# Performance work log

Measured on AMD Instinct MI355X. Metric: run time of the kernel, lower is better.

## Reference

```python
import jax, jax.numpy as jnp
import numpy as np

D = 1024; NHEAD = 8; NQ = 256; B = 8; HM = 64; WM = 64; S = HM * WM; FF = 4 * D
EPS_LN = 1e-5


def _ln(x, g, b):
    m = x.mean(-1, keepdims=True)
    v = ((x - m) ** 2).mean(-1, keepdims=True)
    return (x - m) / jnp.sqrt(v + EPS_LN) * g + b


def _self_attn(x, w_in, b_in, w_out, b_out, nhead):
    # x: [L, B, D] (torch MultiheadAttention, batch_first=False, eval mode)
    L, Bn, Dm = x.shape
    hd = Dm // nhead
    qkv = x @ w_in.T + b_in  # [L, B, 3D]
    q, k, v = jnp.split(qkv, 3, axis=-1)
    sp = lambda t: t.reshape(L, Bn, nhead, hd).transpose(1, 2, 0, 3)  # [B, H, L, hd]
    q, k, v = sp(q), sp(k), sp(v)
    attn = jax.nn.softmax(jnp.einsum('bhqd,bhkd->bhqk', q, k) / float(hd) ** 0.5, axis=-1)
    out = jnp.einsum('bhqk,bhkd->bhqd', attn, v)
    out = out.transpose(2, 0, 1, 3).reshape(L, Bn, Dm)
    return out @ w_out.T + b_out


def setup_inputs() -> dict:
    key = jax.random.key(0)
    ks = iter(jax.random.split(key, 40))
    nrm = lambda shape: jax.random.normal(next(ks), shape, jnp.float32) * 0.02
    return dict(
        query=jax.random.normal(next(ks), (NQ, B, D), jnp.float32),
        memory=jax.random.normal(next(ks), (S, B, D), jnp.float32),
        prev_mask=jax.random.uniform(next(ks), (B, NQ, HM, WM), dtype=jnp.float32),
        h_mem=HM, w_mem=WM,
        sa_in_w=nrm((3 * D, D)), sa_in_b=jnp.zeros((3 * D,), jnp.float32),
        sa_out_w=nrm((D, D)), sa_out_b=jnp.zeros((D,), jnp.float32),
        ln1_g=jnp.ones((D,), jnp.float32), ln1_b=jnp.zeros((D,), jnp.float32),
        ln2_g=jnp.ones((D,), jnp.float32), ln2_b=jnp.zeros((D,), jnp.float32),
        ln3_g=jnp.ones((D,), jnp.float32), ln3_b=jnp.zeros((D,), jnp.float32),
        wq=nrm((D, D)), bq=jnp.zeros((D,), jnp.float32),
        wk=nrm((D, D)), bk=jnp.zeros((D,), jnp.float32),
        wv=nrm((D, D)), bv=jnp.zeros((D,), jnp.float32),
        wo=nrm((D, D)), bo=jnp.zeros((D,), jnp.float32),
        w1=nrm((FF, D)), b1=jnp.zeros((FF,), jnp.float32),
        w2=nrm((D, FF)), b2=jnp.zeros((D,), jnp.float32),
        mask_w=nrm((S, D)), mask_b=jnp.zeros((S,), jnp.float32),
    )


def reference(query, memory, prev_mask, h_mem, w_mem,
              sa_in_w, sa_in_b, sa_out_w, sa_out_b,
              ln1_g, ln1_b, ln2_g, ln2_b, ln3_g, ln3_b,
              wq, bq, wk, bk, wv, bv, wo, bo,
              w1, b1, w2, b2, mask_w, mask_b):
    nq, Bn, d_model = query.shape
    # --- self attention block ---
    q_norm = _ln(query, ln1_g, ln1_b)
    q2 = _self_attn(q_norm, sa_in_w, sa_in_b, sa_out_w, sa_out_b, NHEAD)
    query = query + q2
    # --- masked cross attention (single-head, as in source) ---
    Q = (_ln(query, ln2_g, ln2_b) @ wq.T + bq).transpose(1, 0, 2)  # [B, NQ, D]
    K = (memory @ wk.T + bk).transpose(1, 0, 2)                    # [B, S, D]
    V = (memory @ wv.T + bv).transpose(1, 0, 2)                    # [B, S, D]
    scores = jnp.einsum('bqd,bsd->bqs', Q, K) / float(d_model) ** 0.5
    scores = scores + jnp.log(prev_mask.reshape(Bn, nq, -1) + 1e-6)
    attn = jax.nn.softmax(scores, axis=-1)
    attn_out = jnp.einsum('bqs,bsd->bqd', attn, V).transpose(1, 0, 2)  # [NQ, B, D]
    query = query + (attn_out @ wo.T + bo)
    # --- FFN ---
    h = jax.nn.gelu(_ln(query, ln3_g, ln3_b) @ w1.T + b1, approximate=False)
    query = query + (h @ w2.T + b2)
    # --- mask prediction ---
    q_for_mask = query.transpose(1, 0, 2)                # [B, NQ, D]
    mask_logits = q_for_mask @ mask_w.T + mask_b          # [B, NQ, H*W]
    pred_mask = jax.nn.sigmoid(mask_logits.reshape(Bn, nq, h_mem, w_mem))
    return (query, pred_mask)
```

## Files before the change

### kernel.cpp

```cpp
#include <hip/hip_runtime.h>
#include <cstdint>


typedef __attribute__((ext_vector_type(8))) __bf16 bf16x8;
typedef __attribute__((ext_vector_type(4))) float f32x4;
typedef __attribute__((ext_vector_type(8))) unsigned short ushort8;
typedef __attribute__((ext_vector_type(4))) unsigned short ushort4v;

__device__ __forceinline__ unsigned short f2bf(float f) {
  return __builtin_bit_cast(unsigned short, (__bf16)f);
}

__global__ __launch_bounds__(256) void cast_bf16_kernel(const float* __restrict__ in,
                                                        unsigned short* __restrict__ out,
                                                        int n8) {
  int i = blockIdx.x * 256 + threadIdx.x;
  if (i >= n8) return;
  const float4* p = (const float4*)in + (size_t)i * 2;
  float4 a = p[0], b = p[1];
  ushort8 o;
  o[0] = f2bf(a.x); o[1] = f2bf(a.y); o[2] = f2bf(a.z); o[3] = f2bf(a.w);
  o[4] = f2bf(b.x); o[5] = f2bf(b.y); o[6] = f2bf(b.z); o[7] = f2bf(b.w);
  ((ushort8*)out)[i] = o;
}

__global__ __launch_bounds__(256) void ln_bf16_kernel(const float* __restrict__ x,
                                                      const float* __restrict__ g,
                                                      const float* __restrict__ b,
                                                      unsigned short* __restrict__ out) {
  int row = blockIdx.x, tid = threadIdx.x;
  const float4* xr = (const float4*)(x + (size_t)row * 1024);
  float4 v = xr[tid];
  float s = v.x + v.y + v.z + v.w;
  float sq = v.x * v.x + v.y * v.y + v.z * v.z + v.w * v.w;
#pragma unroll
  for (int o = 32; o > 0; o >>= 1) { s += __shfl_xor(s, o); sq += __shfl_xor(sq, o); }
  __shared__ float red[8];
  int wave = tid >> 6, lane = tid & 63;
  if (lane == 0) { red[wave] = s; red[4 + wave] = sq; }
  __syncthreads();
  float ts = red[0] + red[1] + red[2] + red[3];
  float tq = red[4] + red[5] + red[6] + red[7];
  float mean = ts * (1.f / 1024.f);
  float var = tq * (1.f / 1024.f) - mean * mean;
  float rstd = rsqrtf(var + 1e-5f);
  float4 gv = ((const float4*)g)[tid];
  float4 bv = ((const float4*)b)[tid];
  ushort4v o;
  o[0] = f2bf((v.x - mean) * rstd * gv.x + bv.x);
  o[1] = f2bf((v.y - mean) * rstd * gv.y + bv.y);
  o[2] = f2bf((v.z - mean) * rstd * gv.z + bv.z);
  o[3] = f2bf((v.w - mean) * rstd * gv.w + bv.w);
  ((ushort4v*)(out + (size_t)row * 1024))[tid] = o;
}

template <bool MASK, int CNT>
__global__ __launch_bounds__(256) void softmax_bf16_kernel(const float* __restrict__ sc,
                                                           const float* __restrict__ pm,
                                                           unsigned short* __restrict__ out,
                                                           float scale) {
  const int L = CNT * 256;
  int row = blockIdx.x, tid = threadIdx.x;
  const float* sr = sc + (size_t)row * L;
  float vals[CNT];
  float mx = -1e30f;
#pragma unroll
  for (int i = 0; i < CNT; i++) {
    int idx = tid + (i << 8);
    float v = sr[idx] * scale;
    if (MASK) v += __logf(pm[(size_t)row * L + idx] + 1e-6f);
    vals[i] = v;
    mx = fmaxf(mx, v);
  }
#pragma unroll
  for (int o = 32; o > 0; o >>= 1) mx = fmaxf(mx, __shfl_xor(mx, o));
  __shared__ float red[8];
  int wave = tid >> 6, lane = tid & 63;
  if (lane == 0) red[wave] = mx;
  __syncthreads();
  mx = fmaxf(fmaxf(red[0], red[1]), fmaxf(red[2], red[3]));
  float sum = 0.f;
#pragma unroll
  for (int i = 0; i < CNT; i++) { vals[i] = __expf(vals[i] - mx); sum += vals[i]; }
#pragma unroll
  for (int o = 32; o > 0; o >>= 1) sum += __shfl_xor(sum, o);
  if (lane == 0) red[4 + wave] = sum;
  __syncthreads();
  float rs = 1.f / (red[4] + red[5] + red[6] + red[7]);
#pragma unroll
  for (int i = 0; i < CNT; i++)
    out[(size_t)row * L + tid + (i << 8)] = f2bf(vals[i] * rs);
}

__global__ __launch_bounds__(256) void transpose_bf16_kernel(
    const unsigned short* __restrict__ in, unsigned short* __restrict__ out,
    long in_off, int in_rs, long in_hi, long in_lo, int zdiv,
    long out_off, int out_rs, long out_hi, long out_lo) {
  __shared__ unsigned short t[32][33];
  int z = blockIdx.z;
  int zh = z / zdiv, zl = z % zdiv;
  const unsigned short* ib = in + in_off + (long)zh * in_hi + (long)zl * in_lo;
  unsigned short* ob = out + out_off + (long)zh * out_hi + (long)zl * out_lo;
  int i0 = blockIdx.x * 32;
  int j0 = blockIdx.y * 32;
  int tx = threadIdx.x & 31, ty = threadIdx.x >> 5;
#pragma unroll
  for (int r = ty; r < 32; r += 8) t[r][tx] = ib[(long)(j0 + r) * in_rs + i0 + tx];
  __syncthreads();
#pragma unroll
  for (int r = ty; r < 32; r += 8) ob[(long)(i0 + r) * out_rs + j0 + tx] = t[tx][r];
}

template <bool AF32, bool BIAS, int ACT, bool RES, bool OUTF, bool OUTB>
__global__ __launch_bounds__(256) void gemm_nt_kernel(
    const void* __restrict__ Av, long a_off, int lda, long a_hi, long a_lo,
    const unsigned short* __restrict__ B, long b_off, int ldb, long b_hi, long b_lo,
    const float* __restrict__ bias, const float* __restrict__ Res,
    float* __restrict__ Cf, long c_off, int ldc, long c_hi, long c_lo,
    unsigned short* __restrict__ Cb, long cb_off, int ldcb, long cb_hi, long cb_lo,
    int K, int zdiv) {
  __shared__ unsigned short As[128 * 32];
  __shared__ unsigned short Bs[128 * 32];
  int tid = threadIdx.x;
  int wave = tid >> 6, lane = tid & 63;
  int z = blockIdx.z, zh = z / zdiv, zl = z % zdiv;
  long m0 = (long)blockIdx.x * 128, n0 = (long)blockIdx.y * 128;

  const unsigned short* Bb = B + b_off + zh * b_hi + zl * b_lo + n0 * ldb;
  const unsigned short* Ab16 = nullptr;
  const float* Abf = nullptr;
  if constexpr (AF32)
    Abf = (const float*)Av + a_off + zh * a_hi + zl * a_lo + m0 * lda;
  else
    Ab16 = (const unsigned short*)Av + a_off + zh * a_hi + zl * a_lo + m0 * lda;

  int srow = lane >> 2;
  int scol = (lane & 3) * 8;
  int wm = (wave >> 1) * 64, wn = (wave & 1) * 64;
  int fr = lane & 15;
  int ko = (lane >> 4) * 8;

  f32x4 acc[4][4] = {};

  for (int k0 = 0; k0 < K; k0 += 32) {
    __syncthreads();
    if constexpr (AF32) {
      int row = tid >> 1;
      int cs = (tid & 1) * 16;
      const float* ap = Abf + (long)row * lda + k0 + cs;
      float4 f0 = ((const float4*)ap)[0];
      float4 f1 = ((const float4*)ap)[1];
      float4 f2 = ((const float4*)ap)[2];
      float4 f3 = ((const float4*)ap)[3];
      ushort8 u0, u1;
      u0[0] = f2bf(f0.x); u0[1] = f2bf(f0.y); u0[2] = f2bf(f0.z); u0[3] = f2bf(f0.w);
      u0[4] = f2bf(f1.x); u0[5] = f2bf(f1.y); u0[6] = f2bf(f1.z); u0[7] = f2bf(f1.w);
      u1[0] = f2bf(f2.x); u1[1] = f2bf(f2.y); u1[2] = f2bf(f2.z); u1[3] = f2bf(f2.w);
      u1[4] = f2bf(f3.x); u1[5] = f2bf(f3.y); u1[6] = f2bf(f3.z); u1[7] = f2bf(f3.w);
      ushort8* dst = (ushort8*)(As + row * 32 + cs);
      dst[0] = u0;
      dst[1] = u1;
    } else {
#pragma unroll
      for (int is = 0; is < 2; is++) {
        int rbase = wave * 32 + is * 16;
        const unsigned short* g = Ab16 + (long)(rbase + srow) * lda + k0 + scol;
        __builtin_amdgcn_global_load_lds(
            (const __attribute__((address_space(1))) unsigned int*)g,
            (__attribute__((address_space(3))) unsigned int*)(As + rbase * 32), 16, 0, 0);
      }
    }
#pragma unroll
    for (int is = 0; is < 2; is++) {
      int rbase = wave * 32 + is * 16;
      const unsigned short* g = Bb + (long)(rbase + srow) * ldb + k0 + scol;
      __builtin_amdgcn_global_load_lds(
          (const __attribute__((address_space(1))) unsigned int*)g,
          (__attribute__((address_space(3))) unsigned int*)(Bs + rbase * 32), 16, 0, 0);
    }
    __syncthreads();

    bf16x8 af[4], bfv[4];
#pragma unroll
    for (int i = 0; i < 4; i++)
      af[i] = *(const bf16x8*)(As + (wm + i * 16 + fr) * 32 + ko);
#pragma unroll
    for (int j = 0; j < 4; j++)
      bfv[j] = *(const bf16x8*)(Bs + (wn + j * 16 + fr) * 32 + ko);
#pragma unroll
    for (int i = 0; i < 4; i++)
#pragma unroll
      for (int j = 0; j < 4; j++)
        acc[i][j] = __builtin_amdgcn_mfma_f32_16x16x32_bf16(af[i], bfv[j], acc[i][j], 0, 0, 0);
  }

  long cfo = c_off + zh * c_hi + zl * c_lo;
  long cbo = cb_off + zh * cb_hi + zl * cb_lo;
  int rq = (lane >> 4) * 4;
#pragma unroll
  for (int i = 0; i < 4; i++) {
    long rbase = m0 + wm + i * 16 + rq;
#pragma unroll
    for (int j = 0; j < 4; j++) {
      long cc = n0 + wn + j * 16 + fr;
      float bsv = BIAS ? bias[cc] : 0.f;
#pragma unroll
      for (int r = 0; r < 4; r++) {
        float v = acc[i][j][r] + bsv;
        long ro = rbase + r;
        if constexpr (RES) v += Res[cfo + ro * ldc + cc];
        if constexpr (ACT == 1) v = 0.5f * v * (1.f + erff(v * 0.7071067811865475f));
        if constexpr (ACT == 2) v = 1.f / (1.f + __expf(-v));
        if constexpr (OUTF) Cf[cfo + ro * ldc + cc] = v;
        if constexpr (OUTB) Cb[cbo + ro * ldcb + cc] = f2bf(v);
      }
    }
  }
}

template <bool AF32, bool BIAS, int ACT, bool RES, bool OUTF, bool OUTB>
static void launch_gemm(hipStream_t s, int M, int N, int K, int nz, int zdiv,
                        const void* A, long a_off, int lda, long a_hi, long a_lo,
                        const unsigned short* B, long b_off, int ldb, long b_hi, long b_lo,
                        const float* bias, const float* Res,
                        float* Cf, long c_off, int ldc, long c_hi, long c_lo,
                        unsigned short* Cb, long cb_off, int ldcb, long cb_hi, long cb_lo) {
  dim3 g(M / 128, N / 128, nz);
  gemm_nt_kernel<AF32, BIAS, ACT, RES, OUTF, OUTB><<<g, dim3(256), 0, s>>>(
      A, a_off, lda, a_hi, a_lo, B, b_off, ldb, b_hi, b_lo, bias, Res,
      Cf, c_off, ldc, c_hi, c_lo, Cb, cb_off, ldcb, cb_hi, cb_lo, K, zdiv);
}

static const long WB_SAIN = 0;
static const long WB_SAOUT = 6291456;
static const long WB_WQ = 8388608;
static const long WB_WK = 10485760;
static const long WB_WV = 12582912;
static const long WB_WO = 14680064;
static const long WB_W1 = 16777216;
static const long WB_W2 = 25165824;
static const long WB_MW = 33554432;
static const long OF_K = 41943040;
static const long OF_V = 109051904;
static const long OF_QKV = 176160768;
static const long OF_SC = 188743680;
static const long OF_P = 222298112;
static const long OF_QN = 239075328;
static const long OF_Q = 243269632;
static const long OF_CTX = 247463936;

extern "C" void kernel_launch(void* const* d_in, const int* in_sizes, int n_in,
                              void* d_out, int out_size, void* d_ws, size_t ws_size,
                              hipStream_t stream) {
  (void)in_sizes; (void)n_in; (void)out_size; (void)ws_size;
  const float* query = (const float*)d_in[0];
  const float* memoryp = (const float*)d_in[1];
  const float* prev_mask = (const float*)d_in[2];
  const float* sa_in_w = (const float*)d_in[5];
  const float* sa_in_b = (const float*)d_in[6];
  const float* sa_out_w = (const float*)d_in[7];
  const float* sa_out_b = (const float*)d_in[8];
  const float* ln1_g = (const float*)d_in[9], * ln1_b = (const float*)d_in[10];
  const float* ln2_g = (const float*)d_in[11], * ln2_b = (const float*)d_in[12];
  const float* ln3_g = (const float*)d_in[13], * ln3_b = (const float*)d_in[14];
  const float* wq = (const float*)d_in[15], * bq = (const float*)d_in[16];
  const float* wk = (const float*)d_in[17], * bk = (const float*)d_in[18];
  const float* wv = (const float*)d_in[19], * bv = (const float*)d_in[20];
  const float* wo = (const float*)d_in[21], * bo = (const float*)d_in[22];
  const float* w1 = (const float*)d_in[23], * b1 = (const float*)d_in[24];
  const float* w2 = (const float*)d_in[25], * b2 = (const float*)d_in[26];
  const float* mask_w = (const float*)d_in[27], * mask_b = (const float*)d_in[28];

  uint8_t* ws = (uint8_t*)d_ws;
  auto bf = [&](long off) { return (unsigned short*)(ws + off); };
  auto fp = [&](long off) { return (float*)(ws + off); };
  unsigned short* ZB = nullptr;
  float* ZF = nullptr;

  auto cast = [&](const float* src, long dst, int n) {
    int n8 = n / 8;
    cast_bf16_kernel<<<dim3((n8 + 255) / 256), dim3(256), 0, stream>>>(src, bf(dst), n8);
  };

  cast(sa_in_w, WB_SAIN, 3072 * 1024);
  cast(sa_out_w, WB_SAOUT, 1024 * 1024);
  cast(wq, WB_WQ, 1024 * 1024);
  cast(wk, WB_WK, 1024 * 1024);
  cast(wv, WB_WV, 1024 * 1024);
  cast(wo, WB_WO, 1024 * 1024);
  cast(w1, WB_W1, 4096 * 1024);
  cast(w2, WB_W2, 1024 * 4096);
  cast(mask_w, WB_MW, 4096 * 1024);

  ln_bf16_kernel<<<2048, 256, 0, stream>>>(query, ln1_g, ln1_b, bf(OF_QN));

  launch_gemm<false, true, 0, false, false, true>(stream, 2048, 3072, 1024, 1, 1,
      bf(OF_QN), 0, 1024, 0, 0, bf(WB_SAIN), 0, 1024, 0, 0, sa_in_b, nullptr,
      ZF, 0, 0, 0, 0, bf(OF_QKV), 0, 3072, 0, 0);

  launch_gemm<false, false, 0, false, true, false>(stream, 256, 256, 128, 64, 8,
      bf(OF_QKV), 0, 24576, 3072, 128,
      bf(OF_QKV), 1024, 24576, 3072, 128, nullptr, nullptr,
      fp(OF_SC), 0, 256, 524288, 65536, ZB, 0, 0, 0, 0);

  softmax_bf16_kernel<false, 1><<<16384, 256, 0, stream>>>(
      fp(OF_SC), nullptr, bf(OF_P), 0.08838834764831845f);

  transpose_bf16_kernel<<<dim3(4, 8, 64), 256, 0, stream>>>(
      bf(OF_QKV), bf(OF_QN), 2048L, 24576, 3072L, 128L, 8, 0L, 256, 262144L, 32768L);

  launch_gemm<false, false, 0, false, false, true>(stream, 256, 128, 256, 64, 8,
      bf(OF_P), 0, 256, 524288, 65536,
      bf(OF_QN), 0, 256, 262144, 32768, nullptr, nullptr,
      ZF, 0, 0, 0, 0, bf(OF_CTX), 0, 8192, 1024, 128);

  launch_gemm<false, true, 0, true, true, false>(stream, 2048, 1024, 1024, 1, 1,
      bf(OF_CTX), 0, 1024, 0, 0, bf(WB_SAOUT), 0, 1024, 0, 0, sa_out_b, query,
      fp(OF_QKV), 0, 1024, 0, 0, ZB, 0, 0, 0, 0);

  ln_bf16_kernel<<<2048, 256, 0, stream>>>(fp(OF_QKV), ln2_g, ln2_b, bf(OF_QN));

  launch_gemm<false, true, 0, false, false, true>(stream, 2048, 1024, 1024, 1, 1,
      bf(OF_QN), 0, 1024, 0, 0, bf(WB_WQ), 0, 1024, 0, 0, bq, nullptr,
      ZF, 0, 0, 0, 0, bf(OF_Q), 0, 1024, 0, 0);

  launch_gemm<true, true, 0, false, false, true>(stream, 32768, 1024, 1024, 1, 1,
      memoryp, 0, 1024, 0, 0, bf(WB_WK), 0, 1024, 0, 0, bk, nullptr,
      ZF, 0, 0, 0, 0, bf(OF_K), 0, 1024, 0, 0);
  launch_gemm<true, true, 0, false, false, true>(stream, 32768, 1024, 1024, 1, 1,
      memoryp, 0, 1024, 0, 0, bf(WB_WV), 0, 1024, 0, 0, bv, nullptr,
      ZF, 0, 0, 0, 0, bf(OF_V), 0, 1024, 0, 0);

  launch_gemm<false, false, 0, false, true, false>(stream, 256, 4096, 1024, 8, 1,
      bf(OF_Q), 0, 8192, 1024, 0,
      bf(OF_K), 0, 8192, 1024, 0, nullptr, nullptr,
      fp(OF_SC), 0, 4096, 1048576, 0, ZB, 0, 0, 0, 0);

  softmax_bf16_kernel<true, 16><<<2048, 256, 0, stream>>>(
      fp(OF_SC), prev_mask, bf(OF_P), 0.03125f);

  transpose_bf16_kernel<<<dim3(32, 128, 8), 256, 0, stream>>>(
      bf(OF_V), bf(OF_K), 0L, 8192, 1024L, 0L, 1, 0L, 4096, 4194304L, 0L);

  launch_gemm<false, false, 0, false, false, true>(stream, 256, 1024, 4096, 8, 1,
      bf(OF_P), 0, 4096, 1048576, 0,
      bf(OF_K), 0, 4096, 4194304, 0, nullptr, nullptr,
      ZF, 0, 0, 0, 0, bf(OF_CTX), 0, 8192, 1024, 0);

  launch_gemm<false, true, 0, true, true, false>(stream, 2048, 1024, 1024, 1, 1,
      bf(OF_CTX), 0, 1024, 0, 0, bf(WB_WO), 0, 1024, 0, 0, bo, fp(OF_QKV),
      fp(OF_SC), 0, 1024, 0, 0, ZB, 0, 0, 0, 0);

  ln_bf16_kernel<<<2048, 256, 0, stream>>>(fp(OF_SC), ln3_g, ln3_b, bf(OF_QN));

  launch_gemm<false, true, 1, false, false, true>(stream, 2048, 4096, 1024, 1, 1,
      bf(OF_QN), 0, 1024, 0, 0, bf(WB_W1), 0, 1024, 0, 0, b1, nullptr,
      ZF, 0, 0, 0, 0, bf(OF_P), 0, 4096, 0, 0);

  launch_gemm<false, true, 0, true, true, true>(stream, 2048, 1024, 4096, 1, 1,
      bf(OF_P), 0, 4096, 0, 0, bf(WB_W2), 0, 4096, 0, 0, b2, fp(OF_SC),
      (float*)d_out, 0, 1024, 0, 0, bf(OF_CTX), 0, 1024, 0, 0);

  launch_gemm<false, true, 2, false, true, false>(stream, 256, 4096, 1024, 8, 1,
      bf(OF_CTX), 0, 8192, 1024, 0,
      bf(WB_MW), 0, 1024, 0, 0, mask_b, nullptr,
      (float*)d_out + 2097152, 0, 4096, 1048576, 0, ZB, 0, 0, 0, 0);
}
```

Measured before the change: 1.123 ms.

## Fuse K/V projections, batch weight casts, pre-cast memory, add 64-row GEMM tiles

Replaces the nine weight-cast launches with a single multi-segment cast kernel. The separate K and V projections become one GEMM with N=2048 over concatenated WK|WV weights and a concatenated bias, with the epilogue splitting columns into the K and V buffers. When the workspace is large enough, memory is pre-cast to bf16 so that GEMM can use async global-to-LDS loads instead of converting fp32 in the loop. GEMMs with N=1024 or small grids switch to a 64-row M tile to raise block count. The trade-off is extra workspace, one more pass over memory, and lower per-block reuse on the 64-row tiles.

```diff
diff --git a/kernel.cpp b/kernel.cpp
--- a/kernel.cpp
+++ b/kernel.cpp
@@ -22,6 +22,31 @@
   o[0] = f2bf(a.x); o[1] = f2bf(a.y); o[2] = f2bf(a.z); o[3] = f2bf(a.w);
   o[4] = f2bf(b.x); o[5] = f2bf(b.y); o[6] = f2bf(b.z); o[7] = f2bf(b.w);
   ((ushort8*)out)[i] = o;
+}
+
+struct CastSegs {
+  const float* src[9];
+  int cum[10];
+};
+__global__ __launch_bounds__(256) void cast_multi_kernel(CastSegs cs,
+                                                         unsigned short* __restrict__ out) {
+  int i = blockIdx.x * 256 + threadIdx.x;
+  if (i >= cs.cum[9]) return;
+  int s = 0;
+  while (i >= cs.cum[s + 1]) s++;
+  const float4* p = (const float4*)cs.src[s] + (size_t)(i - cs.cum[s]) * 2;
+  float4 a = p[0], b = p[1];
+  ushort8 o;
+  o[0] = f2bf(a.x); o[1] = f2bf(a.y); o[2] = f2bf(a.z); o[3] = f2bf(a.w);
+  o[4] = f2bf(b.x); o[5] = f2bf(b.y); o[6] = f2bf(b.z); o[7] = f2bf(b.w);
+  ((ushort8*)out)[i] = o;
+}
+
+__global__ __launch_bounds__(256) void bias_concat_kernel(const float* __restrict__ a,
+                                                          const float* __restrict__ b,
+                                                          float* __restrict__ o) {
+  int i = blockIdx.x * 256 + threadIdx.x;
+  o[i] = i < 1024 ? a[i] : b[i - 1024];
 }
 
 __global__ __launch_bounds__(256) void ln_bf16_kernel(const float* __restrict__ x,
@@ -111,7 +136,7 @@
   for (int r = ty; r < 32; r += 8) ob[(long)(i0 + r) * out_rs + j0 + tx] = t[tx][r];
 }
 
-template <bool AF32, bool BIAS, int ACT, bool RES, bool OUTF, bool OUTB>
+template <int TM, bool AF32, bool BIAS, int ACT, bool RES, bool OUTF, bool OUTB, bool KVSPLIT>
 __global__ __launch_bounds__(256) void gemm_nt_kernel(
     const void* __restrict__ Av, long a_off, int lda, long a_hi, long a_lo,
     const unsigned short* __restrict__ B, long b_off, int ldb, long b_hi, long b_lo,
@@ -119,12 +144,13 @@
     float* __restrict__ Cf, long c_off, int ldc, long c_hi, long c_lo,
     unsigned short* __restrict__ Cb, long cb_off, int ldcb, long cb_hi, long cb_lo,
     int K, int zdiv) {
-  __shared__ unsigned short As[128 * 32];
+  constexpr int MI = TM / 32;
+  __shared__ unsigned short As[TM * 32];
   __shared__ unsigned short Bs[128 * 32];
   int tid = threadIdx.x;
   int wave = tid >> 6, lane = tid & 63;
   int z = blockIdx.z, zh = z / zdiv, zl = z % zdiv;
-  long m0 = (long)blockIdx.x * 128, n0 = (long)blockIdx.y * 128;
+  long m0 = (long)blockIdx.x * TM, n0 = (long)blockIdx.y * 128;
 
   const unsigned short* Bb = B + b_off + zh * b_hi + zl * b_lo + n0 * ldb;
   const unsigned short* Ab16 = nullptr;
@@ -136,11 +162,11 @@
 
   int srow = lane >> 2;
   int scol = (lane & 3) * 8;
-  int wm = (wave >> 1) * 64, wn = (wave & 1) * 64;
+  int wm = (wave >> 1) * (TM / 2), wn = (wave & 1) * 64;
   int fr = lane & 15;
   int ko = (lane >> 4) * 8;
 
-  f32x4 acc[4][4] = {};
+  f32x4 acc[MI][4] = {};
 
   for (int k0 = 0; k0 < K; k0 += 32) {
     __syncthreads();
@@ -162,8 +188,8 @@
       dst[1] = u1;
     } else {
 #pragma unroll
-      for (int is = 0; is < 2; is++) {
-        int rbase = wave * 32 + is * 16;
+      for (int is = 0; is < TM / 64; is++) {
+        int rbase = wave * (TM / 4) + is * 16;
         const unsigned short* g = Ab16 + (long)(rbase + srow) * lda + k0 + scol;
         __builtin_amdgcn_global_load_lds(
             (const __attribute__((address_space(1))) unsigned int*)g,
@@ -180,15 +206,15 @@
     }
     __syncthreads();
 
-    bf16x8 af[4], bfv[4];
-#pragma unroll
-    for (int i = 0; i < 4; i++)
+    bf16x8 af[MI], bfv[4];
+#pragma unroll
+    for (int i = 0; i < MI; i++)
       af[i] = *(const bf16x8*)(As + (wm + i * 16 + fr) * 32 + ko);
 #pragma unroll
     for (int j = 0; j < 4; j++)
       bfv[j] = *(const bf16x8*)(Bs + (wn + j * 16 + fr) * 32 + ko);
 #pragma unroll
-    for (int i = 0; i < 4; i++)
+    for (int i = 0; i < MI; i++)
 #pragma unroll
       for (int j = 0; j < 4; j++)
         acc[i][j] = __builtin_amdgcn_mfma_f32_16x16x32_bf16(af[i], bfv[j], acc[i][j], 0, 0, 0);
@@ -198,7 +224,7 @@
   long cbo = cb_off + zh * cb_hi + zl * cb_lo;
   int rq = (lane >> 4) * 4;
 #pragma unroll
-  for (int i = 0; i < 4; i++) {
+  for (int i = 0; i < MI; i++) {
     long rbase = m0 + wm + i * 16 + rq;
 #pragma unroll
     for (int j = 0; j < 4; j++) {
@@ -212,21 +238,24 @@
         if constexpr (ACT == 1) v = 0.5f * v * (1.f + erff(v * 0.7071067811865475f));
         if constexpr (ACT == 2) v = 1.f / (1.f + __expf(-v));
         if constexpr (OUTF) Cf[cfo + ro * ldc + cc] = v;
-        if constexpr (OUTB) Cb[cbo + ro * ldcb + cc] = f2bf(v);
+        if constexpr (OUTB) {
+          long p = KVSPLIT ? ((cc >> 10) * cb_hi + (cc & 1023)) : cc;
+          Cb[cbo + ro * ldcb + p] = f2bf(v);
+        }
       }
     }
   }
 }
 
-template <bool AF32, bool BIAS, int ACT, bool RES, bool OUTF, bool OUTB>
+template <int TM, bool AF32, bool BIAS, int ACT, bool RES, bool OUTF, bool OUTB, bool KVSPLIT = false>
 static void launch_gemm(hipStream_t s, int M, int N, int K, int nz, int zdiv,
                         const void* A, long a_off, int lda, long a_hi, long a_lo,
                         const unsigned short* B, long b_off, int ldb, long b_hi, long b_lo,
                         const float* bias, const float* Res,
                         float* Cf, long c_off, int ldc, long c_hi, long c_lo,
                         unsigned short* Cb, long cb_off, int ldcb, long cb_hi, long cb_lo) {
-  dim3 g(M / 128, N / 128, nz);
-  gemm_nt_kernel<AF32, BIAS, ACT, RES, OUTF, OUTB><<<g, dim3(256), 0, s>>>(
+  dim3 g(M / TM, N / 128, nz);
+  gemm_nt_kernel<TM, AF32, BIAS, ACT, RES, OUTF, OUTB, KVSPLIT><<<g, dim3(256), 0, s>>>(
       A, a_off, lda, a_hi, a_lo, B, b_off, ldb, b_hi, b_lo, bias, Res,
       Cf, c_off, ldc, c_hi, c_lo, Cb, cb_off, ldcb, cb_hi, cb_lo, K, zdiv);
 }
@@ -243,16 +272,19 @@
 static const long OF_K = 41943040;
 static const long OF_V = 109051904;
 static const long OF_QKV = 176160768;
+static const long OF_BKV = 187695104;
 static const long OF_SC = 188743680;
 static const long OF_P = 222298112;
 static const long OF_QN = 239075328;
 static const long OF_Q = 243269632;
 static const long OF_CTX = 247463936;
+static const long OF_MEMBF = 251658240;
+static const size_t FAST_WS = 318767104;
 
 extern "C" void kernel_launch(void* const* d_in, const int* in_sizes, int n_in,
                               void* d_out, int out_size, void* d_ws, size_t ws_size,
                               hipStream_t stream) {
-  (void)in_sizes; (void)n_in; (void)out_size; (void)ws_size;
+  (void)in_sizes; (void)n_in; (void)out_size;
   const float* query = (const float*)d_in[0];
   const float* memoryp = (const float*)d_in[1];
   const float* prev_mask = (const float*)d_in[2];
@@ -276,29 +308,25 @@
   auto fp = [&](long off) { return (float*)(ws + off); };
   unsigned short* ZB = nullptr;
   float* ZF = nullptr;
-
-  auto cast = [&](const float* src, long dst, int n) {
-    int n8 = n / 8;
-    cast_bf16_kernel<<<dim3((n8 + 255) / 256), dim3(256), 0, stream>>>(src, bf(dst), n8);
-  };
-
-  cast(sa_in_w, WB_SAIN, 3072 * 1024);
-  cast(sa_out_w, WB_SAOUT, 1024 * 1024);
-  cast(wq, WB_WQ, 1024 * 1024);
-  cast(wk, WB_WK, 1024 * 1024);
-  cast(wv, WB_WV, 1024 * 1024);
-  cast(wo, WB_WO, 1024 * 1024);
-  cast(w1, WB_W1, 4096 * 1024);
-  cast(w2, WB_W2, 1024 * 4096);
-  cast(mask_w, WB_MW, 4096 * 1024);
+  const bool fast = ws_size >= FAST_WS;
+
+  {
+    CastSegs cs;
+    const float* srcs[9] = {sa_in_w, sa_out_w, wq, wk, wv, wo, w1, w2, mask_w};
+    int n8s[9] = {393216, 131072, 131072, 131072, 131072, 131072, 524288, 524288, 524288};
+    int c = 0;
+    for (int i = 0; i < 9; i++) { cs.src[i] = srcs[i]; cs.cum[i] = c; c += n8s[i]; }
+    cs.cum[9] = c;
+    cast_multi_kernel<<<dim3((c + 255) / 256), dim3(256), 0, stream>>>(cs, bf(0));
+  }
 
   ln_bf16_kernel<<<2048, 256, 0, stream>>>(query, ln1_g, ln1_b, bf(OF_QN));
 
-  launch_gemm<false, true, 0, false, false, true>(stream, 2048, 3072, 1024, 1, 1,
+  launch_gemm<128, false, true, 0, false, false, true>(stream, 2048, 3072, 1024, 1, 1,
       bf(OF_QN), 0, 1024, 0, 0, bf(WB_SAIN), 0, 1024, 0, 0, sa_in_b, nullptr,
       ZF, 0, 0, 0, 0, bf(OF_QKV), 0, 3072, 0, 0);
 
-  launch_gemm<false, false, 0, false, true, false>(stream, 256, 256, 128, 64, 8,
+  launch_gemm<128, false, false, 0, false, true, false>(stream, 256, 256, 128, 64, 8,
       bf(OF_QKV), 0, 24576, 3072, 128,
       bf(OF_QKV), 1024, 24576, 3072, 128, nullptr, nullptr,
       fp(OF_SC), 0, 256, 524288, 65536, ZB, 0, 0, 0, 0);
@@ -309,29 +337,34 @@
   transpose_bf16_kernel<<<dim3(4, 8, 64), 256, 0, stream>>>(
       bf(OF_QKV), bf(OF_QN), 2048L, 24576, 3072L, 128L, 8, 0L, 256, 262144L, 32768L);
 
-  launch_gemm<false, false, 0, false, false, true>(stream, 256, 128, 256, 64, 8,
+  launch_gemm<64, false, false, 0, false, false, true>(stream, 256, 128, 256, 64, 8,
       bf(OF_P), 0, 256, 524288, 65536,
       bf(OF_QN), 0, 256, 262144, 32768, nullptr, nullptr,
       ZF, 0, 0, 0, 0, bf(OF_CTX), 0, 8192, 1024, 128);
 
-  launch_gemm<false, true, 0, true, true, false>(stream, 2048, 1024, 1024, 1, 1,
+  launch_gemm<64, false, true, 0, true, true, false>(stream, 2048, 1024, 1024, 1, 1,
       bf(OF_CTX), 0, 1024, 0, 0, bf(WB_SAOUT), 0, 1024, 0, 0, sa_out_b, query,
       fp(OF_QKV), 0, 1024, 0, 0, ZB, 0, 0, 0, 0);
 
   ln_bf16_kernel<<<2048, 256, 0, stream>>>(fp(OF_QKV), ln2_g, ln2_b, bf(OF_QN));
 
-  launch_gemm<false, true, 0, false, false, true>(stream, 2048, 1024, 1024, 1, 1,
+  launch_gemm<64, false, true, 0, false, false, true>(stream, 2048, 1024, 1024, 1, 1,
       bf(OF_QN), 0, 1024, 0, 0, bf(WB_WQ), 0, 1024, 0, 0, bq, nullptr,
       ZF, 0, 0, 0, 0, bf(OF_Q), 0, 1024, 0, 0);
 
-  launch_gemm<true, true, 0, false, false, true>(stream, 32768, 1024, 1024, 1, 1,
-      memoryp, 0, 1024, 0, 0, bf(WB_WK), 0, 1024, 0, 0, bk, nullptr,
-      ZF, 0, 0, 0, 0, bf(OF_K), 0, 1024, 0, 0);
-  launch_gemm<true, true, 0, false, false, true>(stream, 32768, 1024, 1024, 1, 1,
-      memoryp, 0, 1024, 0, 0, bf(WB_WV), 0, 1024, 0, 0, bv, nullptr,
-      ZF, 0, 0, 0, 0, bf(OF_V), 0, 1024, 0, 0);
-
-  launch_gemm<false, false, 0, false, true, false>(stream, 256, 4096, 1024, 8, 1,
+  bias_concat_kernel<<<8, 256, 0, stream>>>(bk, bv, fp(OF_BKV));
+  if (fast) {
+    cast_bf16_kernel<<<16384, 256, 0, stream>>>(memoryp, bf(OF_MEMBF), 4194304);
+    launch_gemm<128, false, true, 0, false, false, true, true>(stream, 32768, 2048, 1024, 1, 1,
+        bf(OF_MEMBF), 0, 1024, 0, 0, bf(WB_WK), 0, 1024, 0, 0, fp(OF_BKV), nullptr,
+        ZF, 0, 0, 0, 0, bf(OF_K), 0, 1024, 33554432, 0);
+  } else {
+    launch_gemm<128, true, true, 0, false, false, true, true>(stream, 32768, 2048, 1024, 1, 1,
+        memoryp, 0, 1024, 0, 0, bf(WB_WK), 0, 1024, 0, 0, fp(OF_BKV), nullptr,
+        ZF, 0, 0, 0, 0, bf(OF_K), 0, 1024, 33554432, 0);
+  }
+
+  launch_gemm<128, false, false, 0, false, true, false>(stream, 256, 4096, 1024, 8, 1,
       bf(OF_Q), 0, 8192, 1024, 0,
       bf(OF_K), 0, 8192, 1024, 0, nullptr, nullptr,
       fp(OF_SC), 0, 4096, 1048576, 0, ZB, 0, 0, 0, 0);
@@ -342,26 +375,26 @@
   transpose_bf16_kernel<<<dim3(32, 128, 8), 256, 0, stream>>>(
       bf(OF_V), bf(OF_K), 0L, 8192, 1024L, 0L, 1, 0L, 4096, 4194304L, 0L);
 
-  launch_gemm<false, false, 0, false, false, true>(stream, 256, 1024, 4096, 8, 1,
+  launch_gemm<64, false, false, 0, false, false, true>(stream, 256, 1024, 4096, 8, 1,
       bf(OF_P), 0, 4096, 1048576, 0,
       bf(OF_K), 0, 4096, 4194304, 0, nullptr, nullptr,
       ZF, 0, 0, 0, 0, bf(OF_CTX), 0, 8192, 1024, 0);
 
-  launch_gemm<false, true, 0, true, true, false>(stream, 2048, 1024, 1024, 1, 1,
+  launch_gemm<64, false, true, 0, true, true, false>(stream, 2048, 1024, 1024, 1, 1,
       bf(OF_CTX), 0, 1024, 0, 0, bf(WB_WO), 0, 1024, 0, 0, bo, fp(OF_QKV),
       fp(OF_SC), 0, 1024, 0, 0, ZB, 0, 0, 0, 0);
 
   ln_bf16_kernel<<<2048, 256, 0, stream>>>(fp(OF_SC), ln3_g, ln3_b, bf(OF_QN));
 
-  launch_gemm<false, true, 1, false, false, true>(stream, 2048, 4096, 1024, 1, 1,
+  launch_gemm<128, false, true, 1, false, false, true>(stream, 2048, 4096, 1024, 1, 1,
       bf(OF_QN), 0, 1024, 0, 0, bf(WB_W1), 0, 1024, 0, 0, b1, nullptr,
       ZF, 0, 0, 0, 0, bf(OF_P), 0, 4096, 0, 0);
 
-  launch_gemm<false, true, 0, true, true, true>(stream, 2048, 1024, 4096, 1, 1,
+  launch_gemm<64, false, true, 0, true, true, true>(stream, 2048, 1024, 4096, 1, 1,
       bf(OF_P), 0, 4096, 0, 0, bf(WB_W2), 0, 4096, 0, 0, b2, fp(OF_SC),
       (float*)d_out, 0, 1024, 0, 0, bf(OF_CTX), 0, 1024, 0, 0);
 
-  launch_gemm<false, true, 2, false, true, false>(stream, 256, 4096, 1024, 8, 1,
+  launch_gemm<128, false, true, 2, false, true, false>(stream, 256, 4096, 1024, 8, 1,
       bf(OF_CTX), 0, 8192, 1024, 0,
       bf(WB_MW), 0, 1024, 0, 0, mask_b, nullptr,
       (float*)d_out + 2097152, 0, 4096, 1048576, 0, ZB, 0, 0, 0, 0);
```

New measurement: 1.034 ms. 1.09x faster.
